# Performance work log

Hardware: AMD Instinct MI355X
Metric: run time of the kernel (lower is better)

## Reference

```python
import jax, jax.numpy as jnp
import numpy as np

NEG_INF = jnp.finfo(jnp.float32).min


def _continual_mask(attach_test_after, Q, K, test_num, chunk_size):
    """Boolean allowed-mask [B, 1, Q, K] replicating get_continual_mask +
    the per-batch test-query/train-key override in forward()."""
    k_train = K - test_num * chunk_size
    q_train = Q - test_num * chunk_size
    qi = jnp.arange(Q)[:, None]          # [Q,1]
    kj = jnp.arange(K)[None, :]          # [1,K]
    # base causal mask with diagonal offset K-Q (train queries)
    base = kj <= qi + (K - Q)            # [Q,K]
    # block-diagonal tril for test-query / test-key region
    dq = qi - q_train                    # local test row (negative for train rows, unused there)
    dk = kj - k_train
    block = (kj >= k_train) & (dk <= dq) & ((dk // chunk_size) == (dq // chunk_size))
    # per-batch: test query in chunk n may see train keys <= attach_test_after[b, n]
    chunk_idx = jnp.clip(dq[:, 0], 0, None) // chunk_size          # [Q]
    att = attach_test_after[:, chunk_idx]                          # [B,Q]
    train_key_allowed = kj[None, :, :] <= att[:, :, None]          # [B,Q,K]
    allowed = jnp.where(qi < q_train, base[None],
                        jnp.where(kj[None] < k_train, train_key_allowed, block[None]))
    return allowed[:, None]              # [B,1,Q,K]


def setup_inputs() -> dict:
    key = jax.random.key(0)
    k1, k2, k3, k4 = jax.random.split(key, 4)
    B, L, H, D = 4, 2048, 8, 64
    test_num, train_len = 64, 1536
    return {
        "queries": jax.random.normal(k1, (B, L, H, D), dtype=jnp.float32),
        "keys": jax.random.normal(k2, (B, L, H, D), dtype=jnp.float32),
        "values": jax.random.normal(k3, (B, L, H, D), dtype=jnp.float32),
        "attach_test_after": jax.random.randint(k4, (B, test_num), 0, train_len).astype(jnp.int64),
        "train_len": train_len,
    }


def reference(queries, keys, values, attach_test_after, train_len):
    B, Lq, H, Dqk = queries.shape
    test_num = attach_test_after.shape[1]
    chunk_size = (Lq - train_len) // test_num
    q = jnp.transpose(queries, (0, 2, 1, 3))   # [B,H,Lq,D]
    k = jnp.transpose(keys, (0, 2, 1, 3))      # [B,H,Lk,D]
    v = jnp.transpose(values, (0, 2, 1, 3))    # [B,H,Lk,Dv]
    Lk = k.shape[2]
    # vanilla path: scaled QK^T + continual mask + softmax + AV
    logits = jnp.einsum('bhmd,bhnd->bhmn', q, k) / jnp.sqrt(jnp.float32(Dqk))
    allowed = _continual_mask(attach_test_after, Lq, Lk, test_num, chunk_size)
    logits = jnp.where(allowed, logits, NEG_INF)
    attn = jax.nn.softmax(logits, axis=-1)
    out = jnp.einsum('bhmn,bhnd->bhmd', attn, v)
    return out.transpose(0, 2, 1, 3).reshape(B, Lq, H * v.shape[-1])  # b l (h d)
```

## Files before the change

kernel.cpp:

```cpp
#include <hip/hip_runtime.h>
#include <hip/hip_bf16.h>

typedef __bf16 bf16_t;
typedef __bf16 bf16x8 __attribute__((ext_vector_type(8)));
typedef float  f32x4  __attribute__((ext_vector_type(4)));

#define MFMA16(a, b, c) __builtin_amdgcn_mfma_f32_16x16x32_bf16((a), (b), (c), 0, 0, 0)

constexpr int Bc = 4, Lc = 2048, Hc = 8, Dc = 64;
constexpr int HD = Hc * Dc;
constexpr int TRAINc = 1536;
constexpr int ROWS_BLK = 64;
constexpr int KT = 64;
constexpr int PST = 72;

__global__ void prep_k(const float* __restrict__ K, bf16_t* __restrict__ Kb) {
  size_t g = ((size_t)blockIdx.x * 256 + threadIdx.x) * 8;
  float4 a = *(const float4*)(K + g);
  float4 b = *(const float4*)(K + g + 4);
  bf16x8 v;
  v[0] = (bf16_t)a.x; v[1] = (bf16_t)a.y; v[2] = (bf16_t)a.z; v[3] = (bf16_t)a.w;
  v[4] = (bf16_t)b.x; v[5] = (bf16_t)b.y; v[6] = (bf16_t)b.z; v[7] = (bf16_t)b.w;
  *(bf16x8*)(Kb + g) = v;
}

__global__ void prep_v(const float* __restrict__ V, bf16_t* __restrict__ Vt) {
  __shared__ bf16_t T[64][72];
  const int bid = blockIdx.x;
  const int kt = bid & 31, h = (bid >> 5) & 7, b = bid >> 8;
  const int t = (int)threadIdx.x;
  {
    int kl = t >> 2, dp = (t & 3) << 4;
    const float* s = V + ((size_t)(b * Lc + kt * 64 + kl) * Hc + h) * Dc + dp;
    bf16x8 v0, v1;
    float4 f;
    f = *(const float4*)(s);      v0[0]=(bf16_t)f.x; v0[1]=(bf16_t)f.y; v0[2]=(bf16_t)f.z; v0[3]=(bf16_t)f.w;
    f = *(const float4*)(s + 4);  v0[4]=(bf16_t)f.x; v0[5]=(bf16_t)f.y; v0[6]=(bf16_t)f.z; v0[7]=(bf16_t)f.w;
    f = *(const float4*)(s + 8);  v1[0]=(bf16_t)f.x; v1[1]=(bf16_t)f.y; v1[2]=(bf16_t)f.z; v1[3]=(bf16_t)f.w;
    f = *(const float4*)(s + 12); v1[4]=(bf16_t)f.x; v1[5]=(bf16_t)f.y; v1[6]=(bf16_t)f.z; v1[7]=(bf16_t)f.w;
    *(bf16x8*)&T[kl][dp] = v0;
    *(bf16x8*)&T[kl][dp + 8] = v1;
  }
  __syncthreads();
  {
    int d = t >> 2, kp = (t & 3) << 4;
    bf16x8 o0, o1;
#pragma unroll
    for (int i = 0; i < 8; ++i) { o0[i] = T[kp + i][d]; o1[i] = T[kp + 8 + i][d]; }
    bf16_t* dst = Vt + ((size_t)((b * Hc + h) * Dc + d)) * Lc + kt * 64 + kp;
    *(bf16x8*)dst = o0;
    *(bf16x8*)(dst + 8) = o1;
  }
}

static __device__ __forceinline__ void load16(const bf16_t* g, bf16_t* l) {
  __builtin_amdgcn_global_load_lds(
      (const __attribute__((address_space(1))) unsigned int*)g,
      (__attribute__((address_space(3))) unsigned int*)l, 16, 0, 0);
}

__global__ __launch_bounds__(256, 2)
void continual_attn(const float* __restrict__ Qg, const bf16_t* __restrict__ Kb,
                    const bf16_t* __restrict__ Vt, const int* __restrict__ ATT,
                    float* __restrict__ OUT)
{
  __shared__ __align__(16) bf16_t Klds[2][KT * 64];
  __shared__ __align__(16) bf16_t Vlds[2][Dc * KT];
  __shared__ __align__(16) bf16_t Plds[4][16 * PST];

  const int bid  = blockIdx.x;
  const int qblk = 31 - (bid >> 5);
  const int h    = bid & 7;
  const int b    = (bid >> 3) & 3;
  const int q0   = qblk * ROWS_BLK;

  const int tid  = (int)threadIdx.x;
  const int wave = tid >> 6;
  const int lane = tid & 63;
  const int quad = lane >> 4;
  const int col  = lane & 15;
  const int qw   = q0 + wave * 16;

  const size_t bhQ = (size_t)b * Lc * HD + (size_t)h * Dc;

  const int kr = tid >> 3;
  const bf16_t* ksrcA = Kb + bhQ + (size_t)kr * HD + (((tid & 7) ^ (kr & 7)) << 3);
  const bf16_t* vsrcA = Vt + ((size_t)((b * Hc + h) * Dc + kr)) * Lc + (((tid & 7) ^ (kr & 7)) << 3);
  const bf16_t* vsrcB = vsrcA + (size_t)32 * Lc;

  bf16x8 aq[2];
  {
    const float* qp = Qg + bhQ + (size_t)(qw + col) * HD + quad * 8;
#pragma unroll
    for (int t = 0; t < 2; ++t) {
      float4 lo = *(const float4*)(qp + t * 32);
      float4 hi = *(const float4*)(qp + t * 32 + 4);
      bf16x8 v;
      v[0] = (bf16_t)(lo.x * 0.125f); v[1] = (bf16_t)(lo.y * 0.125f);
      v[2] = (bf16_t)(lo.z * 0.125f); v[3] = (bf16_t)(lo.w * 0.125f);
      v[4] = (bf16_t)(hi.x * 0.125f); v[5] = (bf16_t)(hi.y * 0.125f);
      v[6] = (bf16_t)(hi.z * 0.125f); v[7] = (bf16_t)(hi.w * 0.125f);
      aq[t] = v;
    }
  }

  const bool testblk = (q0 >= TRAINc);
  int kend[4], cstart[4], qir[4];
#pragma unroll
  for (int r = 0; r < 4; ++r) {
    int qi = qw + quad * 4 + r;
    qir[r] = qi;
    if (testblk) {
      kend[r]   = ATT[b * 64 + ((qi - TRAINc) >> 3)] + 1;
      cstart[r] = qi & ~7;
    } else {
      kend[r]   = qi + 1;
      cstart[r] = 0;
    }
  }

  int ntA, ndiag, kfull_end;
  if (testblk) {
    int c0 = (q0 - TRAINc) >> 3;
    int amax = 0, amin = 0x7fffffff;
#pragma unroll
    for (int i = 0; i < 8; ++i) {
      int a = ATT[b * 64 + c0 + i];
      amax = (a > amax) ? a : amax;
      amin = (a < amin) ? a : amin;
    }
    ntA = (amax >> 6) + 1;
    ndiag = 1;
    kfull_end = amin + 1;
  } else {
    ntA = qblk + 1;
    ndiag = 0;
    kfull_end = q0 + 1;
  }
  const int ntot = ntA + ndiag;

  float lsumL[4] = {0.f, 0.f, 0.f, 0.f};
  f32x4 o[4] = {{0,0,0,0},{0,0,0,0},{0,0,0,0},{0,0,0,0}};

  const int cA = ((quad ^ (col & 7)) << 3);

  {
    bf16_t* kd = Klds[0];
    bf16_t* vd = Vlds[0];
    load16(ksrcA, kd + wave * 512);
    load16(ksrcA + (size_t)32 * HD, kd + 2048 + wave * 512);
    load16(vsrcA, vd + wave * 512);
    load16(vsrcB, vd + 2048 + wave * 512);
  }

  for (int ti = 0; ti < ntot; ++ti) {
    const int buf = ti & 1;
    __syncthreads();

    if (ti + 1 < ntot) {
      const int kn = (ti + 1 < ntA) ? (ti + 1) * KT : q0 + (ti + 1 - ntA) * KT;
      bf16_t* kd = Klds[1 - buf];
      bf16_t* vd = Vlds[1 - buf];
      load16(ksrcA + (size_t)kn * HD, kd + wave * 512);
      load16(ksrcA + (size_t)(kn + 32) * HD, kd + 2048 + wave * 512);
      load16(vsrcA + kn, vd + wave * 512);
      load16(vsrcB + kn, vd + 2048 + wave * 512);
    }

    const bf16_t* kb = Klds[buf];
    const bf16_t* vbuf = Vlds[buf];
    const int k0 = (ti < ntA) ? ti * KT : q0 + (ti - ntA) * KT;

    f32x4 sf[4] = {{0,0,0,0},{0,0,0,0},{0,0,0,0},{0,0,0,0}};
#pragma unroll
    for (int kg = 0; kg < 4; ++kg) {
      const bf16_t* krow = kb + (kg * 16 + col) * 64;
      bf16x8 k0f = *(const bf16x8*)(krow + cA);
      bf16x8 k1f = *(const bf16x8*)(krow + (cA ^ 32));
      sf[kg] = MFMA16(aq[0], k0f, sf[kg]);
      sf[kg] = MFMA16(aq[1], k1f, sf[kg]);
    }

    const int mode = (ti >= ntA) ? 2 : ((k0 + KT <= kfull_end) ? 0 : 1);
    if (mode == 1) {
#pragma unroll
      for (int kg = 0; kg < 4; ++kg) {
        const int kgv = k0 + kg * 16 + col;
#pragma unroll
        for (int r = 0; r < 4; ++r)
          if (kgv >= kend[r]) sf[kg][r] = -1e30f;
      }
    } else if (mode == 2) {
#pragma unroll
      for (int kg = 0; kg < 4; ++kg) {
        const int kgv = k0 + kg * 16 + col;
#pragma unroll
        for (int r = 0; r < 4; ++r)
          if (kgv < cstart[r] || kgv > qir[r]) sf[kg][r] = -1e30f;
      }
    }

    bf16_t* pw = Plds[wave];
#pragma unroll
    for (int kg = 0; kg < 4; ++kg) {
#pragma unroll
      for (int r = 0; r < 4; ++r) {
        float p = __expf(sf[kg][r]);
        lsumL[r] += p;
        pw[(quad * 4 + r) * PST + kg * 16 + col] = (bf16_t)p;
      }
    }
    bf16x8 pa0 = *(const bf16x8*)&pw[col * PST + quad * 8];
    bf16x8 pa1 = *(const bf16x8*)&pw[col * PST + 32 + quad * 8];

#pragma unroll
    for (int t = 0; t < 4; ++t) {
      const bf16_t* vrow = vbuf + (t * 16 + col) * 64;
      bf16x8 v0 = *(const bf16x8*)(vrow + cA);
      bf16x8 v1 = *(const bf16x8*)(vrow + (cA ^ 32));
      o[t] = MFMA16(pa0, v0, o[t]);
      o[t] = MFMA16(pa1, v1, o[t]);
    }
  }

#pragma unroll
  for (int r = 0; r < 4; ++r) {
    float rs = lsumL[r];
    rs += __shfl_xor(rs, 1);
    rs += __shfl_xor(rs, 2);
    rs += __shfl_xor(rs, 4);
    rs += __shfl_xor(rs, 8);
    float inv = 1.f / rs;
    int qi = qw + quad * 4 + r;
    float* op = OUT + ((size_t)b * Lc + qi) * HD + (size_t)h * Dc + col;
    op[0]  = o[0][r] * inv;
    op[16] = o[1][r] * inv;
    op[32] = o[2][r] * inv;
    op[48] = o[3][r] * inv;
  }
}

extern "C" void kernel_launch(void* const* d_in, const int* in_sizes, int n_in,
                              void* d_out, int out_size, void* d_ws, size_t ws_size,
                              hipStream_t stream) {
  const float* Q   = (const float*)d_in[0];
  const float* K   = (const float*)d_in[1];
  const float* V   = (const float*)d_in[2];
  const int*   ATT = (const int*)d_in[3];
  float* OUT = (float*)d_out;
  (void)in_sizes; (void)n_in; (void)out_size; (void)ws_size;

  const size_t NE = (size_t)Bc * Lc * Hc * Dc;
  bf16_t* Kb = (bf16_t*)d_ws;
  bf16_t* Vt = Kb + NE;

  prep_k<<<dim3((unsigned)(NE / 8 / 256)), dim3(256), 0, stream>>>(K, Kb);
  prep_v<<<dim3(Bc * Hc * (Lc / 64)), dim3(256), 0, stream>>>(V, Vt);
  continual_attn<<<dim3(Bc * Hc * (Lc / ROWS_BLK)), dim3(256), 0, stream>>>(Q, Kb, Vt, ATT, OUT);
}
```

Before: 131.5 us.

## Split key range across blocks with atomic accumulation and separate normalization

Splits each query block's key range into up to four 512-key chunks handled by separate workgroups, giving 80 partitions per batch-head instead of 32 with uneven causal work. Partial outputs and row sums are accumulated with float atomics into a zeroed workspace, and a new kernel divides by the sums. It also swizzles the P scratch layout to drop LDS padding and raises the occupancy hint. In exchange it adds a memset, atomic traffic, an extra pass over the output, and run-to-run nondeterminism in the accumulated values.

After: 152.9 us. 16.3% more time.

```diff
diff --git a/kernel.cpp b/kernel.cpp
--- a/kernel.cpp
+++ b/kernel.cpp
@@ -10,9 +10,8 @@
 constexpr int Bc = 4, Lc = 2048, Hc = 8, Dc = 64;
 constexpr int HD = Hc * Dc;
 constexpr int TRAINc = 1536;
-constexpr int ROWS_BLK = 64;
 constexpr int KT = 64;
-constexpr int PST = 72;
+constexpr int PST = 64;
 
 __global__ void prep_k(const float* __restrict__ K, bf16_t* __restrict__ Kb) {
   size_t g = ((size_t)blockIdx.x * 256 + threadIdx.x) * 8;
@@ -59,20 +58,25 @@
       (__attribute__((address_space(3))) unsigned int*)l, 16, 0, 0);
 }
 
-__global__ __launch_bounds__(256, 2)
+__global__ __launch_bounds__(256, 4)
 void continual_attn(const float* __restrict__ Qg, const bf16_t* __restrict__ Kb,
                     const bf16_t* __restrict__ Vt, const int* __restrict__ ATT,
-                    float* __restrict__ OUT)
+                    float* __restrict__ Oacc, float* __restrict__ Lsum)
 {
   __shared__ __align__(16) bf16_t Klds[2][KT * 64];
   __shared__ __align__(16) bf16_t Vlds[2][Dc * KT];
   __shared__ __align__(16) bf16_t Plds[4][16 * PST];
 
-  const int bid  = blockIdx.x;
-  const int qblk = 31 - (bid >> 5);
-  const int h    = bid & 7;
-  const int b    = (bid >> 3) & 3;
-  const int q0   = qblk * ROWS_BLK;
+  const int bid = blockIdx.x;
+  const int pid = bid >> 5;
+  const int bh  = bid & 31;
+  const int b   = bh >> 3, h = bh & 7;
+  int qblk, ck;
+  if (pid < 8)       { qblk = pid;                 ck = 0; }
+  else if (pid < 24) { qblk = 8 + ((pid - 8) >> 1);  ck = (pid - 8) & 1; }
+  else if (pid < 48) { int t = pid - 24; int q3 = t / 3; qblk = 16 + q3; ck = t - 3 * q3; }
+  else               { int t = pid - 48; qblk = 24 + (t >> 2); ck = t & 3; }
+  const int q0 = qblk * 64;
 
   const int tid  = (int)threadIdx.x;
   const int wave = tid >> 6;
@@ -80,6 +84,45 @@
   const int quad = lane >> 4;
   const int col  = lane & 15;
   const int qw   = q0 + wave * 16;
+
+  const bool testblk = (q0 >= TRAINc);
+  int kend[4], cstart[4], qir[4];
+#pragma unroll
+  for (int r = 0; r < 4; ++r) {
+    int qi = qw + quad * 4 + r;
+    qir[r] = qi;
+    if (testblk) {
+      kend[r]   = ATT[b * 64 + ((qi - TRAINc) >> 3)] + 1;
+      cstart[r] = qi & ~7;
+    } else {
+      kend[r]   = qi + 1;
+      cstart[r] = 0;
+    }
+  }
+
+  int kbeg, ntiles, kfull_end, diag = 0;
+  if (!testblk) {
+    kbeg = ck * 512;
+    int ke = min(kbeg + 512, q0 + 64);
+    ntiles = (ke - kbeg) >> 6;
+    kfull_end = q0 + 1;
+  } else if (ck == 3) {
+    kbeg = q0; ntiles = 1; diag = 1; kfull_end = 0;
+  } else {
+    int c0 = (q0 - TRAINc) >> 3;
+    int amax = 0, amin = 0x7fffffff;
+#pragma unroll
+    for (int i = 0; i < 8; ++i) {
+      int a = ATT[b * 64 + c0 + i];
+      amax = (a > amax) ? a : amax;
+      amin = (a < amin) ? a : amin;
+    }
+    kbeg = ck * 512;
+    int ke = min(kbeg + 512, amax + 1);
+    if (ke <= kbeg) return;
+    ntiles = (ke - kbeg + 63) >> 6;
+    kfull_end = amin + 1;
+  }
 
   const size_t bhQ = (size_t)b * Lc * HD + (size_t)h * Dc;
 
@@ -104,72 +147,30 @@
     }
   }
 
-  const bool testblk = (q0 >= TRAINc);
-  int kend[4], cstart[4], qir[4];
-#pragma unroll
-  for (int r = 0; r < 4; ++r) {
-    int qi = qw + quad * 4 + r;
-    qir[r] = qi;
-    if (testblk) {
-      kend[r]   = ATT[b * 64 + ((qi - TRAINc) >> 3)] + 1;
-      cstart[r] = qi & ~7;
-    } else {
-      kend[r]   = qi + 1;
-      cstart[r] = 0;
-    }
-  }
-
-  int ntA, ndiag, kfull_end;
-  if (testblk) {
-    int c0 = (q0 - TRAINc) >> 3;
-    int amax = 0, amin = 0x7fffffff;
-#pragma unroll
-    for (int i = 0; i < 8; ++i) {
-      int a = ATT[b * 64 + c0 + i];
-      amax = (a > amax) ? a : amax;
-      amin = (a < amin) ? a : amin;
-    }
-    ntA = (amax >> 6) + 1;
-    ndiag = 1;
-    kfull_end = amin + 1;
-  } else {
-    ntA = qblk + 1;
-    ndiag = 0;
-    kfull_end = q0 + 1;
-  }
-  const int ntot = ntA + ndiag;
-
   float lsumL[4] = {0.f, 0.f, 0.f, 0.f};
   f32x4 o[4] = {{0,0,0,0},{0,0,0,0},{0,0,0,0},{0,0,0,0}};
-
   const int cA = ((quad ^ (col & 7)) << 3);
 
-  {
-    bf16_t* kd = Klds[0];
-    bf16_t* vd = Vlds[0];
-    load16(ksrcA, kd + wave * 512);
-    load16(ksrcA + (size_t)32 * HD, kd + 2048 + wave * 512);
-    load16(vsrcA, vd + wave * 512);
-    load16(vsrcB, vd + 2048 + wave * 512);
-  }
-
-  for (int ti = 0; ti < ntot; ++ti) {
+  load16(ksrcA + (size_t)kbeg * HD, Klds[0] + wave * 512);
+  load16(ksrcA + (size_t)(kbeg + 32) * HD, Klds[0] + 2048 + wave * 512);
+  load16(vsrcA + kbeg, Vlds[0] + wave * 512);
+  load16(vsrcB + kbeg, Vlds[0] + 2048 + wave * 512);
+
+  for (int ti = 0; ti < ntiles; ++ti) {
     const int buf = ti & 1;
     __syncthreads();
 
-    if (ti + 1 < ntot) {
-      const int kn = (ti + 1 < ntA) ? (ti + 1) * KT : q0 + (ti + 1 - ntA) * KT;
-      bf16_t* kd = Klds[1 - buf];
-      bf16_t* vd = Vlds[1 - buf];
-      load16(ksrcA + (size_t)kn * HD, kd + wave * 512);
-      load16(ksrcA + (size_t)(kn + 32) * HD, kd + 2048 + wave * 512);
-      load16(vsrcA + kn, vd + wave * 512);
-      load16(vsrcB + kn, vd + 2048 + wave * 512);
+    if (ti + 1 < ntiles) {
+      const int kn = kbeg + (ti + 1) * KT;
+      load16(ksrcA + (size_t)kn * HD, Klds[1 - buf] + wave * 512);
+      load16(ksrcA + (size_t)(kn + 32) * HD, Klds[1 - buf] + 2048 + wave * 512);
+      load16(vsrcA + kn, Vlds[1 - buf] + wave * 512);
+      load16(vsrcB + kn, Vlds[1 - buf] + 2048 + wave * 512);
     }
 
     const bf16_t* kb = Klds[buf];
     const bf16_t* vbuf = Vlds[buf];
-    const int k0 = (ti < ntA) ? ti * KT : q0 + (ti - ntA) * KT;
+    const int k0 = kbeg + ti * KT;
 
     f32x4 sf[4] = {{0,0,0,0},{0,0,0,0},{0,0,0,0},{0,0,0,0}};
 #pragma unroll
@@ -181,7 +182,7 @@
       sf[kg] = MFMA16(aq[1], k1f, sf[kg]);
     }
 
-    const int mode = (ti >= ntA) ? 2 : ((k0 + KT <= kfull_end) ? 0 : 1);
+    const int mode = diag ? 2 : ((k0 + KT <= kfull_end) ? 0 : 1);
     if (mode == 1) {
 #pragma unroll
       for (int kg = 0; kg < 4; ++kg) {
@@ -207,11 +208,12 @@
       for (int r = 0; r < 4; ++r) {
         float p = __expf(sf[kg][r]);
         lsumL[r] += p;
-        pw[(quad * 4 + r) * PST + kg * 16 + col] = (bf16_t)p;
+        const int row = quad * 4 + r;
+        pw[row * PST + (((kg * 2 + (col >> 3)) ^ (row & 7)) << 3) + (col & 7)] = (bf16_t)p;
       }
     }
-    bf16x8 pa0 = *(const bf16x8*)&pw[col * PST + quad * 8];
-    bf16x8 pa1 = *(const bf16x8*)&pw[col * PST + 32 + quad * 8];
+    bf16x8 pa0 = *(const bf16x8*)&pw[col * PST + cA];
+    bf16x8 pa1 = *(const bf16x8*)&pw[col * PST + (cA ^ 32)];
 
 #pragma unroll
     for (int t = 0; t < 4; ++t) {
@@ -230,14 +232,30 @@
     rs += __shfl_xor(rs, 2);
     rs += __shfl_xor(rs, 4);
     rs += __shfl_xor(rs, 8);
-    float inv = 1.f / rs;
     int qi = qw + quad * 4 + r;
-    float* op = OUT + ((size_t)b * Lc + qi) * HD + (size_t)h * Dc + col;
-    op[0]  = o[0][r] * inv;
-    op[16] = o[1][r] * inv;
-    op[32] = o[2][r] * inv;
-    op[48] = o[3][r] * inv;
-  }
+    float* op = Oacc + ((size_t)b * Lc + qi) * HD + (size_t)h * Dc + col;
+    unsafeAtomicAdd(op,      o[0][r]);
+    unsafeAtomicAdd(op + 16, o[1][r]);
+    unsafeAtomicAdd(op + 32, o[2][r]);
+    unsafeAtomicAdd(op + 48, o[3][r]);
+    if (col == 0)
+      unsafeAtomicAdd(&Lsum[((size_t)b * Hc + h) * Lc + qi], rs);
+  }
+}
+
+__global__ void norm_out(const float* __restrict__ Oacc, const float* __restrict__ Lsum,
+                         float* __restrict__ OUT) {
+  size_t i = ((size_t)blockIdx.x * 256 + threadIdx.x) * 8;
+  int b = (int)(i >> 20);
+  int l = (int)(i >> 9) & 2047;
+  int h = (int)(i >> 6) & 7;
+  float inv = 1.f / Lsum[((size_t)b * Hc + h) * Lc + l];
+  float4 a = *(const float4*)(Oacc + i);
+  float4 c = *(const float4*)(Oacc + i + 4);
+  a.x *= inv; a.y *= inv; a.z *= inv; a.w *= inv;
+  c.x *= inv; c.y *= inv; c.z *= inv; c.w *= inv;
+  *(float4*)(OUT + i)     = a;
+  *(float4*)(OUT + i + 4) = c;
 }
 
 extern "C" void kernel_launch(void* const* d_in, const int* in_sizes, int n_in,
@@ -251,10 +269,14 @@
   (void)in_sizes; (void)n_in; (void)out_size; (void)ws_size;
 
   const size_t NE = (size_t)Bc * Lc * Hc * Dc;
-  bf16_t* Kb = (bf16_t*)d_ws;
-  bf16_t* Vt = Kb + NE;
-
+  bf16_t* Kb   = (bf16_t*)d_ws;
+  bf16_t* Vt   = Kb + NE;
+  float*  Oacc = (float*)(Vt + NE);
+  float*  Lsum = Oacc + NE;
+
+  hipMemsetAsync(Oacc, 0, (NE + (size_t)Bc * Hc * Lc) * sizeof(float), stream);
   prep_k<<<dim3((unsigned)(NE / 8 / 256)), dim3(256), 0, stream>>>(K, Kb);
   prep_v<<<dim3(Bc * Hc * (Lc / 64)), dim3(256), 0, stream>>>(V, Vt);
-  continual_attn<<<dim3(Bc * Hc * (Lc / ROWS_BLK)), dim3(256), 0, stream>>>(Q, Kb, Vt, ATT, OUT);
-}
+  continual_attn<<<dim3(80 * 32), dim3(256), 0, stream>>>(Q, Kb, Vt, ATT, Oacc, Lsum);
+  norm_out<<<dim3((unsigned)(NE / 8 / 256)), dim3(256), 0, stream>>>(Oacc, Lsum, OUT);
+}
```
